# Performance work log

Hardware: AMD Instinct MI355X
Metric: run time of the kernel (lower is better)

The kernel has to match this reference:

```python
import jax, jax.numpy as jnp
import numpy as np

N_HEAD = 12
N_EMBD = 768
HEAD_DIM = N_EMBD // N_HEAD
B, S = 4, 2048


def setup_inputs() -> dict:
    key = jax.random.key(0)
    k1, k2, k3, k4, k5 = jax.random.split(key, 5)
    x = jax.random.normal(k1, (B, S, N_EMBD), dtype=jnp.float32)
    # causal additive mask: 1.0 where attention is disallowed (strictly upper triangle)
    mask = (1.0 - jnp.tril(jnp.ones((S, S), dtype=jnp.float32)))[None, None, :, :]
    scale = 0.02
    W_attn = jax.random.normal(k2, (N_EMBD, 3 * N_EMBD), dtype=jnp.float32) * scale
    b_attn = jnp.zeros((3 * N_EMBD,), dtype=jnp.float32)
    W_proj = jax.random.normal(k3, (N_EMBD, N_EMBD), dtype=jnp.float32) * scale
    b_proj = jnp.zeros((N_EMBD,), dtype=jnp.float32)
    return {"x": x, "mask": mask, "W_attn": W_attn, "b_attn": b_attn,
            "W_proj": W_proj, "b_proj": b_proj}


def reference(x, mask, W_attn, b_attn, W_proj, b_proj):
    Bn, Sn, _ = x.shape
    qkv = x @ W_attn + b_attn                      # [B,S,3E]
    q, k, v = jnp.split(qkv, 3, axis=-1)           # each [B,S,E]

    def heads(t):
        return t.reshape(Bn, Sn, N_HEAD, HEAD_DIM).transpose(0, 2, 1, 3)  # [B,H,S,D]

    q, k, v = heads(q), heads(k), heads(v)
    attn = jnp.einsum('bhqd,bhkd->bhqk', q, k) / jnp.sqrt(jnp.float32(HEAD_DIM))
    attn = attn + mask * (-1e9)
    attn = jax.nn.softmax(attn, axis=-1)
    # dropout in inference mode = identity
    out = jnp.einsum('bhqk,bhkd->bhqd', attn, v)   # [B,H,S,D]
    out = out.transpose(0, 2, 1, 3).reshape(Bn, Sn, N_EMBD)
    return out @ W_proj + b_proj
```

## Files before the change

kernel.cpp:

```cpp
#include <hip/hip_runtime.h>
#include <stdint.h>

#define NHEAD 12
#define HDIM  64
#define EMB   768
#define N3    2304
#define SEQ   2048
#define BATCH 4
#define MROWS 8192

#define QSCALE 0.18033688011112042f

typedef __bf16 bf16_t;
typedef __bf16 bf16x8 __attribute__((ext_vector_type(8)));
typedef __bf16 bf16x4 __attribute__((ext_vector_type(4)));
typedef short  s16x4  __attribute__((ext_vector_type(4)));
typedef float  f32x4  __attribute__((ext_vector_type(4)));

__device__ __forceinline__ void gld_lds16(void* lds, const void* g) {
    __builtin_amdgcn_global_load_lds((const __attribute__((address_space(1))) void*)g,
                                     (__attribute__((address_space(3))) void*)lds,
                                     16, 0, 0);
}

__device__ __forceinline__ float fast_exp2(float x) {
    return __builtin_amdgcn_exp2f(x);
}

__device__ __forceinline__ f32x4 mfma16_bf16(bf16x4 a, bf16x4 b, f32x4 c) {
#if __has_builtin(__builtin_amdgcn_mfma_f32_16x16x16_bf16)
    return __builtin_amdgcn_mfma_f32_16x16x16_bf16(a, b, c, 0, 0, 0);
#else
    union U { bf16x4 h; s16x4 s; };
    U ua, ub; ua.h = a; ub.h = b;
    return __builtin_amdgcn_mfma_f32_16x16x16bf16_1k(ua.s, ub.s, c, 0, 0, 0);
#endif
}

__global__ __launch_bounds__(256) void prep_kernel(
    const float* __restrict__ Wa, bf16_t* __restrict__ WaT,
    const float* __restrict__ Wp, bf16_t* __restrict__ WpT,
    const float* __restrict__ x,  bf16_t* __restrict__ xb)
{
    __shared__ float tile[32][33];
    const int bid = blockIdx.x;
    if (bid < 2304) {
        const float* W; bf16_t* WT; int K, N, b;
        if (bid < 1728) { W = Wa; WT = WaT; K = 768; N = 2304; b = bid; }
        else            { W = Wp; WT = WpT; K = 768; N = 768;  b = bid - 1728; }
        const int nb = N / 32;
        const int n0 = (b % nb) * 32, k0 = (b / nb) * 32;
        const int tx = threadIdx.x & 31, ty = threadIdx.x >> 5;
#pragma unroll
        for (int i = 0; i < 32; i += 8)
            tile[ty + i][tx] = W[(size_t)(k0 + ty + i) * N + (n0 + tx)];
        __syncthreads();
#pragma unroll
        for (int i = 0; i < 32; i += 8)
            WT[(size_t)(n0 + ty + i) * K + (k0 + tx)] = (bf16_t)tile[tx][ty + i];
    } else {
        const int n8 = MROWS * EMB / 8;
        int idx    = (bid - 2304) * 256 + threadIdx.x;
        const int stride = 1536 * 256;
        for (int i = idx; i < n8; i += stride) {
            float4 a = ((const float4*)x)[i * 2];
            float4 b = ((const float4*)x)[i * 2 + 1];
            bf16x8 v;
            v[0] = (bf16_t)a.x; v[1] = (bf16_t)a.y; v[2] = (bf16_t)a.z; v[3] = (bf16_t)a.w;
            v[4] = (bf16_t)b.x; v[5] = (bf16_t)b.y; v[6] = (bf16_t)b.z; v[7] = (bf16_t)b.w;
            ((bf16x8*)xb)[i] = v;
        }
    }
}

template<int MODE>
__global__ __launch_bounds__(256) void gemm_kernel(
    const bf16_t* __restrict__ Av,
    const bf16_t* __restrict__ BT,
    const float* __restrict__ bias,
    float* __restrict__ out,
    bf16_t* __restrict__ qbuf,
    bf16_t* __restrict__ kbuf,
    bf16_t* __restrict__ vbuf,
    int Ncols)
{
    const int K = 768;
    __shared__ alignas(16) bf16_t As[2][128 * 32];
    __shared__ alignas(16) bf16_t Bs[2][128 * 32];

    const int tid    = threadIdx.x;
    const int wave   = tid >> 6;
    const int lane   = tid & 63;
    const int lane15 = lane & 15;
    const int quad   = lane >> 4;

    const int bid   = blockIdx.x;
    const int chunk = (int)(gridDim.x >> 3);
    const int swz   = (bid & 7) * chunk + (bid >> 3);
    const int NB    = Ncols >> 7;
    const int mBase = (swz / NB) * 128;
    const int nBase = (swz % NB) * 128;

    const int wm = (wave >> 1) * 64;
    const int wn = (wave & 1) * 64;

    f32x4 acc[4][4];
#pragma unroll
    for (int i = 0; i < 4; i++)
#pragma unroll
        for (int j = 0; j < 4; j++) acc[i][j] = (f32x4){0.f, 0.f, 0.f, 0.f};

    const bf16_t* aSrc = Av + (size_t)mBase * K;
    const bf16_t* bSrc = BT + (size_t)nBase * K;

    const int srow = lane >> 2;
    const int sch  = lane & 3;

    auto issueA = [&](int k0, int buf) {
#pragma unroll
        for (int p = 0; p < 2; p++) {
            int r0  = p * 64 + wave * 16;
            int row = r0 + srow;
            int lch = sch ^ (row & 3);
            gld_lds16(&As[buf][r0 * 32], aSrc + (size_t)row * K + k0 + lch * 8);
        }
    };
    auto issueB = [&](int k0, int buf) {
#pragma unroll
        for (int p = 0; p < 2; p++) {
            int r0  = p * 64 + wave * 16;
            int row = r0 + srow;
            int lch = sch ^ (row & 3);
            gld_lds16(&Bs[buf][r0 * 32], bSrc + (size_t)row * K + k0 + lch * 8);
        }
    };

    issueA(0, 0);
    issueB(0, 0);

    for (int k0 = 0, it = 0; k0 < K; k0 += 32, it++) {
        const int buf = it & 1;
        __syncthreads();
        if (k0 + 32 < K) {
            issueB(k0 + 32, buf ^ 1);
            issueA(k0 + 32, buf ^ 1);
        }

        bf16x8 aF[4], bF[4];
#pragma unroll
        for (int t = 0; t < 4; t++) {
            int ra = wm + t * 16 + lane15;
            int rb = wn + t * 16 + lane15;
            aF[t] = *(const bf16x8*)&As[buf][ra * 32 + (quad ^ (ra & 3)) * 8];
            bF[t] = *(const bf16x8*)&Bs[buf][rb * 32 + (quad ^ (rb & 3)) * 8];
        }
#pragma unroll
        for (int i = 0; i < 4; i++)
#pragma unroll
            for (int j = 0; j < 4; j++)
                acc[i][j] = __builtin_amdgcn_mfma_f32_16x16x32_bf16(aF[i], bF[j], acc[i][j], 0, 0, 0);
    }

    const int region = nBase / EMB;
#pragma unroll
    for (int i = 0; i < 4; i++) {
#pragma unroll
        for (int j = 0; j < 4; j++) {
            int gn = nBase + wn + j * 16 + lane15;
            float bv = bias[gn];
            if (region == 2) {
                int within = gn - 2 * EMB;
                int h = within >> 6, d = within & 63;
                int gm0 = mBase + wm + i * 16 + quad * 4;
                int b = gm0 >> 11, s = gm0 & 2047;
                int bh = b * NHEAD + h;
                bf16x4 v4;
#pragma unroll
                for (int r = 0; r < 4; r++) v4[r] = (bf16_t)(acc[i][j][r] + bv);
                *(bf16x4*)&vbuf[((size_t)bh * HDIM + d) * SEQ + s] = v4;
            } else {
                bf16_t* dst = (region == 0) ? qbuf : kbuf;
                const float scale = (region == 0) ? QSCALE : 1.0f;
                int within = gn - region * EMB;
                int h = within >> 6, d = within & 63;
#pragma unroll
                for (int r = 0; r < 4; r++) {
                    int gm = mBase + wm + i * 16 + quad * 4 + r;
                    int b = gm >> 11, s = gm & 2047;
                    int bh = b * NHEAD + h;
                    dst[((size_t)bh * SEQ + s) * HDIM + d] = (bf16_t)((acc[i][j][r] + bv) * scale);
                }
            }
        }
    }
}

__global__ __launch_bounds__(256) void proj_kernel(
    const bf16_t* __restrict__ Av,
    const bf16_t* __restrict__ BT,
    const float*  __restrict__ bias,
    float* __restrict__ out)
{
    const int K = 768;
    __shared__ alignas(16) bf16_t As[2][64 * 64];
    __shared__ alignas(16) bf16_t Bs[2][128 * 64];

    const int tid    = threadIdx.x;
    const int wave   = tid >> 6;
    const int lane   = tid & 63;
    const int lane15 = lane & 15;
    const int quad   = lane >> 4;

    const int bid   = blockIdx.x;
    const int swz   = (bid & 7) * 96 + (bid >> 3);
    const int mBase = (swz / 6) * 64;
    const int nBase = (swz % 6) * 128;

    f32x4 acc[4][2];
#pragma unroll
    for (int t = 0; t < 4; t++)
#pragma unroll
        for (int u = 0; u < 2; u++) acc[t][u] = (f32x4){0.f, 0.f, 0.f, 0.f};

    const bf16_t* aSrc = Av + (size_t)mBase * K;
    const bf16_t* bSrc = BT + (size_t)nBase * K;

    const int srow8 = lane >> 3;
    const int sch8  = lane & 7;

    auto issueA = [&](int k0, int buf) {
#pragma unroll
        for (int p = 0; p < 2; p++) {
            int r0  = wave * 8 + p * 32;
            int row = r0 + srow8;
            int lch = sch8 ^ (row & 7);
            gld_lds16(&As[buf][r0 * 64], aSrc + (size_t)row * K + k0 + lch * 8);
        }
    };
    auto issueB = [&](int k0, int buf) {
#pragma unroll
        for (int p = 0; p < 4; p++) {
            int r0  = wave * 8 + p * 32;
            int row = r0 + srow8;
            int lch = sch8 ^ (row & 7);
            gld_lds16(&Bs[buf][r0 * 64], bSrc + (size_t)row * K + k0 + lch * 8);
        }
    };

    issueA(0, 0);
    issueB(0, 0);

    for (int k0 = 0, it = 0; k0 < K; k0 += 64, it++) {
        const int buf = it & 1;
        __syncthreads();
        if (k0 + 64 < K) {
            issueB(k0 + 64, buf ^ 1);
            issueA(k0 + 64, buf ^ 1);
        }

        bf16x8 aF[2][4], bF[2][2];
#pragma unroll
        for (int kk = 0; kk < 2; kk++) {
#pragma unroll
            for (int t = 0; t < 4; t++) {
                int ra = t * 16 + lane15;
                aF[kk][t] = *(const bf16x8*)&As[buf][ra * 64 + (((quad + kk * 4) ^ (ra & 7)) * 8)];
            }
#pragma unroll
            for (int u = 0; u < 2; u++) {
                int rb = wave * 32 + u * 16 + lane15;
                bF[kk][u] = *(const bf16x8*)&Bs[buf][rb * 64 + (((quad + kk * 4) ^ (rb & 7)) * 8)];
            }
        }
#pragma unroll
        for (int kk = 0; kk < 2; kk++)
#pragma unroll
            for (int t = 0; t < 4; t++)
#pragma unroll
                for (int u = 0; u < 2; u++)
                    acc[t][u] = __builtin_amdgcn_mfma_f32_16x16x32_bf16(aF[kk][t], bF[kk][u], acc[t][u], 0, 0, 0);
    }

#pragma unroll
    for (int t = 0; t < 4; t++) {
#pragma unroll
        for (int u = 0; u < 2; u++) {
            int gn = nBase + wave * 32 + u * 16 + lane15;
            float bv = bias[gn];
#pragma unroll
            for (int r = 0; r < 4; r++) {
                int gm = mBase + t * 16 + quad * 4 + r;
                out[(size_t)gm * EMB + gn] = acc[t][u][r] + bv;
            }
        }
    }
}

__global__ __launch_bounds__(256) void attn_kernel(
    const bf16_t* __restrict__ qbuf,
    const bf16_t* __restrict__ kbuf,
    const bf16_t* __restrict__ vtbuf,
    bf16_t* __restrict__ obuf)
{
    __shared__ alignas(16) bf16_t Ks[2][64 * 64];
    __shared__ alignas(16) bf16_t Vs[2][64 * 64];
    __shared__ alignas(16) bf16_t Plds[4][16 * 72];

    const int tid    = threadIdx.x;
    const int wave   = tid >> 6;
    const int lane   = tid & 63;
    const int lane15 = lane & 15;
    const int quad   = lane >> 4;

    const int bid = blockIdx.x;
    const int swz = (bid & 7) * 96 + (bid >> 3);
    const int bh = swz >> 4;
    const int j  = swz & 15;

    const bf16_t* Qp = qbuf  + (size_t)bh * SEQ * HDIM;
    const bf16_t* Kp = kbuf  + (size_t)bh * SEQ * HDIM;
    const bf16_t* Vp = vtbuf + (size_t)bh * HDIM * SEQ;
    bf16_t* pl = &Plds[wave][0];
    const int b = bh / NHEAD, h = bh % NHEAD;

    const int srow8 = lane >> 3;
    const int sch8  = lane & 7;

    auto issueKV = [&](int kb, int buf) {
#pragma unroll
        for (int p = 0; p < 2; p++) {
            int r0  = p * 32 + wave * 8;
            int row = r0 + srow8;
            int lch = sch8 ^ (row & 7);
            gld_lds16(&Ks[buf][r0 * 64], Kp + (size_t)(kb + row) * HDIM + lch * 8);
            gld_lds16(&Vs[buf][r0 * 64], Vp + (size_t)row * SEQ + kb + lch * 8);
        }
    };

    const int q0s[2] = { j * 64 + wave * 16, (31 - j) * 64 + wave * 16 };

    bf16x8 qf[2][2];
#pragma unroll
    for (int qq = 0; qq < 2; qq++) {
        qf[qq][0] = *(const bf16x8*)&Qp[(size_t)(q0s[qq] + lane15) * HDIM + quad * 8];
        qf[qq][1] = *(const bf16x8*)&Qp[(size_t)(q0s[qq] + lane15) * HDIM + 32 + quad * 8];
    }

    float lrow[2] = {0.f, 0.f};
    f32x4 oT[2][4];
#pragma unroll
    for (int qq = 0; qq < 2; qq++)
#pragma unroll
        for (int t = 0; t < 4; t++) oT[qq][t] = (f32x4){0.f, 0.f, 0.f, 0.f};

    const int nT = 32 - j;
    issueKV(0, 0);

    for (int kt = 0; kt < nT; kt++) {
        const int buf = kt & 1;
        __syncthreads();
        if (kt + 1 < nT) issueKV((kt + 1) * 64, buf ^ 1);

        const int kb = kt * 64;

#pragma unroll
        for (int qq = 0; qq < 2; qq++) {
            const int q0q = q0s[qq];
            if (qq == 0 && kt > j) continue;

            f32x4 sT[4];
            __builtin_amdgcn_s_setprio(1);
#pragma unroll
            for (int kg = 0; kg < 4; kg++) {
                sT[kg] = (f32x4){0.f, 0.f, 0.f, 0.f};
                int row = kg * 16 + lane15;
                bf16x8 kf0 = *(const bf16x8*)&Ks[buf][row * 64 + ((quad    ) ^ (row & 7)) * 8];
                bf16x8 kf1 = *(const bf16x8*)&Ks[buf][row * 64 + ((quad + 4) ^ (row & 7)) * 8];
                sT[kg] = __builtin_amdgcn_mfma_f32_16x16x32_bf16(kf0, qf[qq][0], sT[kg], 0, 0, 0);
                sT[kg] = __builtin_amdgcn_mfma_f32_16x16x32_bf16(kf1, qf[qq][1], sT[kg], 0, 0, 0);
            }
            __builtin_amdgcn_s_setprio(0);

            if (kb + 64 > q0q) {
                const int query = q0q + lane15;
#pragma unroll
                for (int kg = 0; kg < 4; kg++) {
                    int key0 = kb + kg * 16 + quad * 4;
#pragma unroll
                    for (int r = 0; r < 4; r++)
                        sT[kg][r] = (key0 + r <= query) ? sT[kg][r] : -1e30f;
                }
            }

            bf16x4 pf[4];
#pragma unroll
            for (int kg = 0; kg < 4; kg++) {
#pragma unroll
                for (int r = 0; r < 4; r++) sT[kg][r] = fast_exp2(sT[kg][r]);
                lrow[qq] += (sT[kg][0] + sT[kg][1]) + (sT[kg][2] + sT[kg][3]);
                bf16x4 v;
#pragma unroll
                for (int r = 0; r < 4; r++) v[r] = (bf16_t)sT[kg][r];
                pf[kg] = v;
            }

            __builtin_amdgcn_s_setprio(1);
#pragma unroll
            for (int t = 0; t < 4; t++) {
                int vrow = t * 16 + lane15;
#pragma unroll
                for (int kg = 0; kg < 4; kg++) {
                    int c    = kg * 2 + (quad >> 1);
                    int phys = c ^ (vrow & 7);
                    bf16x4 vf = *(const bf16x4*)&Vs[buf][vrow * 64 + phys * 8 + (quad & 1) * 4];
                    oT[qq][t] = mfma16_bf16(vf, pf[kg], oT[qq][t]);
                }
            }
            __builtin_amdgcn_s_setprio(0);
        }
    }

#pragma unroll
    for (int qq = 0; qq < 2; qq++) {
        const int q0q = q0s[qq];
        float l = lrow[qq];
        l += __shfl_xor(l, 16, 64);
        l += __shfl_xor(l, 32, 64);
        const float inv = 1.0f / l;

#pragma unroll
        for (int t = 0; t < 4; t++)
#pragma unroll
            for (int r = 0; r < 4; r++)
                pl[lane15 * 72 + t * 16 + quad * 4 + r] = (bf16_t)(oT[qq][t][r] * inv);

        const int qrow = lane >> 2;
        const int ch   = lane & 3;
        bf16_t* orow = &obuf[((size_t)(b * SEQ + q0q + qrow)) * EMB + h * HDIM];
#pragma unroll
        for (int p = 0; p < 2; p++) {
            bf16x8 v = *(const bf16x8*)&pl[qrow * 72 + (ch + p * 4) * 8];
            *(bf16x8*)&orow[(ch + p * 4) * 8] = v;
        }
    }
}

extern "C" void kernel_launch(void* const* d_in, const int* in_sizes, int n_in,
                              void* d_out, int out_size, void* d_ws, size_t ws_size,
                              hipStream_t stream) {
    const float* x      = (const float*)d_in[0];
    const float* W_attn = (const float*)d_in[2];
    const float* b_attn = (const float*)d_in[3];
    const float* W_proj = (const float*)d_in[4];
    const float* b_proj = (const float*)d_in[5];
    float* out = (float*)d_out;

    bf16_t* ws  = (bf16_t*)d_ws;
    bf16_t* WaT = ws;
    bf16_t* WpT = WaT + (size_t)N3 * EMB;
    bf16_t* Qb  = WpT + (size_t)EMB * EMB;
    bf16_t* Kb  = Qb + (size_t)BATCH * NHEAD * SEQ * HDIM;
    bf16_t* Vt  = Kb + (size_t)BATCH * NHEAD * SEQ * HDIM;
    bf16_t* Ob  = Vt + (size_t)BATCH * NHEAD * SEQ * HDIM;
    bf16_t* xb  = Ob;

    prep_kernel<<<3840, 256, 0, stream>>>(W_attn, WaT, W_proj, WpT, x, xb);

    gemm_kernel<1><<<1152, 256, 0, stream>>>(
        xb, WaT, b_attn, nullptr, Qb, Kb, Vt, N3);

    attn_kernel<<<768, 256, 0, stream>>>(Qb, Kb, Vt, Ob);

    proj_kernel<<<768, 256, 0, stream>>>(Ob, WpT, b_proj, out);
}
```

Baseline: 217.1 us.

## Stage two KV tiles per barrier and hoist K fragments out of query loop

The attention loop now loads 128 keys (two 64-key tiles) per double-buffer stage, halving the number of __syncthreads barriers and prefetch issues per block. K fragments are read from LDS once per tile and reused for both query groups instead of being reloaded per query group. This doubles LDS use for K/V (to 64KB), which may reduce occupancy, and adds registers for the hoisted K fragments.

```diff
diff --git a/kernel.cpp b/kernel.cpp
--- a/kernel.cpp
+++ b/kernel.cpp
@@ -302,8 +302,8 @@
     const bf16_t* __restrict__ vtbuf,
     bf16_t* __restrict__ obuf)
 {
-    __shared__ alignas(16) bf16_t Ks[2][64 * 64];
-    __shared__ alignas(16) bf16_t Vs[2][64 * 64];
+    __shared__ alignas(16) bf16_t Ks[2][2][64 * 64];
+    __shared__ alignas(16) bf16_t Vs[2][2][64 * 64];
     __shared__ alignas(16) bf16_t Plds[4][16 * 72];
 
     const int tid    = threadIdx.x;
@@ -326,14 +326,18 @@
     const int srow8 = lane >> 3;
     const int sch8  = lane & 7;
 
-    auto issueKV = [&](int kb, int buf) {
-#pragma unroll
-        for (int p = 0; p < 2; p++) {
-            int r0  = p * 32 + wave * 8;
-            int row = r0 + srow8;
-            int lch = sch8 ^ (row & 7);
-            gld_lds16(&Ks[buf][r0 * 64], Kp + (size_t)(kb + row) * HDIM + lch * 8);
-            gld_lds16(&Vs[buf][r0 * 64], Vp + (size_t)row * SEQ + kb + lch * 8);
+    auto issueKV = [&](int kbp, int buf) {
+#pragma unroll
+        for (int hh = 0; hh < 2; hh++) {
+            const int kb = kbp + hh * 64;
+#pragma unroll
+            for (int p = 0; p < 2; p++) {
+                int r0  = p * 32 + wave * 8;
+                int row = r0 + srow8;
+                int lch = sch8 ^ (row & 7);
+                gld_lds16(&Ks[buf][hh][r0 * 64], Kp + (size_t)(kb + row) * HDIM + lch * 8);
+                gld_lds16(&Vs[buf][hh][r0 * 64], Vp + (size_t)row * SEQ + kb + lch * 8);
+            }
         }
     };
 
@@ -354,69 +358,80 @@
         for (int t = 0; t < 4; t++) oT[qq][t] = (f32x4){0.f, 0.f, 0.f, 0.f};
 
     const int nT = 32 - j;
+    const int nP = (nT + 1) >> 1;
     issueKV(0, 0);
 
-    for (int kt = 0; kt < nT; kt++) {
-        const int buf = kt & 1;
+    for (int ktp = 0; ktp < nP; ktp++) {
+        const int buf = ktp & 1;
         __syncthreads();
-        if (kt + 1 < nT) issueKV((kt + 1) * 64, buf ^ 1);
-
-        const int kb = kt * 64;
-
-#pragma unroll
-        for (int qq = 0; qq < 2; qq++) {
-            const int q0q = q0s[qq];
-            if (qq == 0 && kt > j) continue;
-
-            f32x4 sT[4];
-            __builtin_amdgcn_s_setprio(1);
+        if (ktp + 1 < nP) issueKV((ktp + 1) * 128, buf ^ 1);
+
+#pragma unroll
+        for (int half = 0; half < 2; half++) {
+            const int kt = ktp * 2 + half;
+            if (kt >= nT) continue;
+            const int kb = kt * 64;
+
+            bf16x8 kf[4][2];
 #pragma unroll
             for (int kg = 0; kg < 4; kg++) {
-                sT[kg] = (f32x4){0.f, 0.f, 0.f, 0.f};
                 int row = kg * 16 + lane15;
-                bf16x8 kf0 = *(const bf16x8*)&Ks[buf][row * 64 + ((quad    ) ^ (row & 7)) * 8];
-                bf16x8 kf1 = *(const bf16x8*)&Ks[buf][row * 64 + ((quad + 4) ^ (row & 7)) * 8];
-                sT[kg] = __builtin_amdgcn_mfma_f32_16x16x32_bf16(kf0, qf[qq][0], sT[kg], 0, 0, 0);
-                sT[kg] = __builtin_amdgcn_mfma_f32_16x16x32_bf16(kf1, qf[qq][1], sT[kg], 0, 0, 0);
-            }
-            __builtin_amdgcn_s_setprio(0);
-
-            if (kb + 64 > q0q) {
-                const int query = q0q + lane15;
+                kf[kg][0] = *(const bf16x8*)&Ks[buf][half][row * 64 + ((quad    ) ^ (row & 7)) * 8];
+                kf[kg][1] = *(const bf16x8*)&Ks[buf][half][row * 64 + ((quad + 4) ^ (row & 7)) * 8];
+            }
+
+#pragma unroll
+            for (int qq = 0; qq < 2; qq++) {
+                const int q0q = q0s[qq];
+                if (qq == 0 && kt > j) continue;
+
+                f32x4 sT[4];
+                __builtin_amdgcn_s_setprio(1);
 #pragma unroll
                 for (int kg = 0; kg < 4; kg++) {
-                    int key0 = kb + kg * 16 + quad * 4;
-#pragma unroll
-                    for (int r = 0; r < 4; r++)
-                        sT[kg][r] = (key0 + r <= query) ? sT[kg][r] : -1e30f;
+                    sT[kg] = (f32x4){0.f, 0.f, 0.f, 0.f};
+                    sT[kg] = __builtin_amdgcn_mfma_f32_16x16x32_bf16(kf[kg][0], qf[qq][0], sT[kg], 0, 0, 0);
+                    sT[kg] = __builtin_amdgcn_mfma_f32_16x16x32_bf16(kf[kg][1], qf[qq][1], sT[kg], 0, 0, 0);
                 }
-            }
-
-            bf16x4 pf[4];
-#pragma unroll
-            for (int kg = 0; kg < 4; kg++) {
-#pragma unroll
-                for (int r = 0; r < 4; r++) sT[kg][r] = fast_exp2(sT[kg][r]);
-                lrow[qq] += (sT[kg][0] + sT[kg][1]) + (sT[kg][2] + sT[kg][3]);
-                bf16x4 v;
-#pragma unroll
-                for (int r = 0; r < 4; r++) v[r] = (bf16_t)sT[kg][r];
-                pf[kg] = v;
-            }
-
-            __builtin_amdgcn_s_setprio(1);
-#pragma unroll
-            for (int t = 0; t < 4; t++) {
-                int vrow = t * 16 + lane15;
+                __builtin_amdgcn_s_setprio(0);
+
+                if (kb + 64 > q0q) {
+                    const int query = q0q + lane15;
+#pragma unroll
+                    for (int kg = 0; kg < 4; kg++) {
+                        int key0 = kb + kg * 16 + quad * 4;
+#pragma unroll
+                        for (int r = 0; r < 4; r++)
+                            sT[kg][r] = (key0 + r <= query) ? sT[kg][r] : -1e30f;
+                    }
+                }
+
+                bf16x4 pf[4];
 #pragma unroll
                 for (int kg = 0; kg < 4; kg++) {
-                    int c    = kg * 2 + (quad >> 1);
-                    int phys = c ^ (vrow & 7);
-                    bf16x4 vf = *(const bf16x4*)&Vs[buf][vrow * 64 + phys * 8 + (quad & 1) * 4];
-                    oT[qq][t] = mfma16_bf16(vf, pf[kg], oT[qq][t]);
+#pragma unroll
+                    for (int r = 0; r < 4; r++) sT[kg][r] = fast_exp2(sT[kg][r]);
+                    lrow[qq] += (sT[kg][0] + sT[kg][1]) + (sT[kg][2] + sT[kg][3]);
+                    bf16x4 v;
+#pragma unroll
+                    for (int r = 0; r < 4; r++) v[r] = (bf16_t)sT[kg][r];
+                    pf[kg] = v;
                 }
-            }
-            __builtin_amdgcn_s_setprio(0);
+
+                __builtin_amdgcn_s_setprio(1);
+#pragma unroll
+                for (int t = 0; t < 4; t++) {
+                    int vrow = t * 16 + lane15;
+#pragma unroll
+                    for (int kg = 0; kg < 4; kg++) {
+                        int c    = kg * 2 + (quad >> 1);
+                        int phys = c ^ (vrow & 7);
+                        bf16x4 vf = *(const bf16x4*)&Vs[buf][half][vrow * 64 + phys * 8 + (quad & 1) * 4];
+                        oT[qq][t] = mfma16_bf16(vf, pf[kg], oT[qq][t]);
+                    }
+                }
+                __builtin_amdgcn_s_setprio(0);
+            }
         }
     }
 
```

Result: slower. 229.6 us (+5.8%).
